# Kernel tuning notes

Hardware: AMD Instinct MI355X
Metric: run time of the kernel (lower is better)

## Reference

```python
import jax, jax.numpy as jnp
import numpy as np

HIDDEN = 4096
NH = 32          # num attention heads
NKV = 8          # num key/value heads
HD = HIDDEN // NH  # 128
THETA = 10000.0
WINDOW = 4096    # sliding window hard-coded in forward


def _rotate_half(x):
    x1, x2 = jnp.split(x, 2, axis=-1)
    return jnp.concatenate((-x2, x1), axis=-1)


def setup_inputs() -> dict:
    key = jax.random.key(0)
    ks = jax.random.split(key, 5)
    B, S = 1, 2048
    hidden_states = jax.random.normal(ks[0], (B, S, HIDDEN), jnp.float32)
    position_ids = jnp.broadcast_to(jnp.arange(S, dtype=jnp.int64), (B, S))
    s = 0.02
    q_w = jax.random.normal(ks[1], (HIDDEN, NH * HD), jnp.float32) * s
    k_w = jax.random.normal(ks[2], (HIDDEN, NKV * HD), jnp.float32) * s
    v_w = jax.random.normal(ks[3], (HIDDEN, NKV * HD), jnp.float32) * s
    o_w = jax.random.normal(ks[4], (NH * HD, HIDDEN), jnp.float32) * s
    return {"hidden_states": hidden_states, "position_ids": position_ids,
            "q_w": q_w, "k_w": k_w, "v_w": v_w, "o_w": o_w}


def reference(hidden_states, position_ids, q_w, k_w, v_w, o_w):
    B, S, _ = hidden_states.shape
    # projections (bias=False), split heads -> [B, H, S, D]
    q = (hidden_states @ q_w).reshape(B, S, NH, HD).transpose(0, 2, 1, 3)
    k = (hidden_states @ k_w).reshape(B, S, NKV, HD).transpose(0, 2, 1, 3)
    v = (hidden_states @ v_w).reshape(B, S, NKV, HD).transpose(0, 2, 1, 3)

    # rotary embedding cache (MistralRotaryEmbedding)
    inv_freq = 1.0 / (THETA ** (jnp.arange(0, HD, 2, dtype=jnp.float32) / HD))
    t = jnp.arange(S, dtype=jnp.float32)
    freqs = t[:, None] * inv_freq[None, :]           # [S, HD/2]
    emb = jnp.concatenate((freqs, freqs), axis=-1)   # [S, HD]
    cos = jnp.cos(emb)[position_ids][:, None]        # [B, 1, S, HD]
    sin = jnp.sin(emb)[position_ids][:, None]
    q = q * cos + _rotate_half(q) * sin
    k = k * cos + _rotate_half(k) * sin

    # GQA repeat_kv: [B, NKV, S, D] -> [B, NH, S, D]
    rep = NH // NKV
    k = jnp.repeat(k, rep, axis=1)
    v = jnp.repeat(v, rep, axis=1)

    # scores + sliding-window causal mask
    scale = 1.0 / np.sqrt(HD).astype(np.float32)
    w = jnp.einsum("bhqd,bhkd->bhqk", q, k) * scale  # [B, NH, S, S]
    i = jnp.arange(S)[:, None]
    j = jnp.arange(S)[None, :]
    allowed = (j <= i) & ((i - j) < WINDOW)
    neg = jnp.finfo(jnp.float32).min
    w = w + jnp.where(allowed, 0.0, neg)[None, None]

    # fp32 softmax (upcast as in HF Mistral)
    w = jax.nn.softmax(w.astype(jnp.float32), axis=-1).astype(q.dtype)

    out = jnp.einsum("bhqk,bhkd->bhqd", w, v)        # [B, NH, S, D]
    out = out.transpose(0, 2, 1, 3).reshape(B, S, NH * HD)
    return out @ o_w                                  # [B, S, HIDDEN]
```

## Files before the change

### kernel.cpp

```cpp
#include <hip/hip_runtime.h>
#include <hip/hip_bf16.h>

#define S 2048
#define HID 4096
#define NH 32
#define NKV 8
#define HD 128
#define QKVN 6144

typedef __attribute__((ext_vector_type(8))) short bf16x8;
typedef __attribute__((ext_vector_type(4))) float f32x4;
typedef __attribute__((ext_vector_type(8))) unsigned short u16x8;
typedef __attribute__((ext_vector_type(4))) unsigned short u16x4;

#define GLOAD16(src, dst)                                                        \
  __builtin_amdgcn_global_load_lds(                                              \
      (const __attribute__((address_space(1))) unsigned int*)(src),              \
      (__attribute__((address_space(3))) unsigned int*)(dst), 16, 0, 0)

__device__ __forceinline__ unsigned short f2bf(float f) {
  union { float f; unsigned u; } c; c.f = f;
  unsigned u = c.u;
  return (unsigned short)((u + 0x7FFFu + ((u >> 16) & 1u)) >> 16);
}
__device__ __forceinline__ float bf2f(unsigned short h) {
  union { unsigned u; float f; } c; c.u = ((unsigned)h) << 16;
  return c.f;
}

__global__ void convert_kernel(const float* __restrict__ in,
                               unsigned short* __restrict__ out, int n4) {
  int i = blockIdx.x * blockDim.x + threadIdx.x;
  if (i < n4) {
    float4 v = ((const float4*)in)[i];
    ushort4 o;
    o.x = f2bf(v.x); o.y = f2bf(v.y); o.z = f2bf(v.z); o.w = f2bf(v.w);
    ((ushort4*)out)[i] = o;
  }
}

__global__ void transpose_convert(const float* __restrict__ in,
                                  unsigned short* __restrict__ out, int N) {
  __shared__ float tile[32][33];
  int tx = threadIdx.x, ty = threadIdx.y;
  int n0 = blockIdx.x * 32, k0 = blockIdx.y * 32;
#pragma unroll
  for (int i = 0; i < 32; i += 8)
    tile[ty + i][tx] = in[(size_t)(k0 + ty + i) * N + n0 + tx];
  __syncthreads();
#pragma unroll
  for (int i = 0; i < 32; i += 8)
    out[(size_t)(n0 + ty + i) * HID + k0 + tx] = f2bf(tile[tx][ty + i]);
}

__device__ __forceinline__ void storeC(unsigned short* C, size_t idx, float v) { C[idx] = f2bf(v); }
__device__ __forceinline__ void storeC(float* C, size_t idx, float v) { C[idx] = v; }

template <typename OutT>
__launch_bounds__(256, 2)
__global__ void gemm_bt(const unsigned short* __restrict__ A,
                        const unsigned short* __restrict__ Bt,
                        OutT* __restrict__ C, int K, int ldc) {
  __shared__ unsigned short As[2][2][128 * 32];
  __shared__ unsigned short Bs[2][2][128 * 32];
  const int tid = threadIdx.x, lane = tid & 63, w = tid >> 6;
  const int wr = w >> 1, wc = w & 1;
  const int m0 = blockIdx.y * 128, n0 = blockIdx.x * 128;
  const int lq = lane & 15, g = lane >> 4;
  const int swz8 = (g ^ (lq & 3) ^ ((lq >> 2) & 3)) << 3;

  f32x4 acc[4][4] = {};
  const int NT = K >> 6;

  auto STAGE_PAIR = [&](int bb, int ss, int kt) {
#pragma unroll
    for (int i = 0; i < 2; ++i) {
      int ci = tid + i * 256;
      int row = ci >> 2;
      int jl = (((ci & 3) ^ (row & 3) ^ ((row >> 2) & 3))) << 3;
      GLOAD16(A + (size_t)(m0 + row) * K + kt + ss * 32 + jl, &As[bb][ss][ci * 8]);
      GLOAD16(Bt + (size_t)(n0 + row) * K + kt + ss * 32 + jl, &Bs[bb][ss][ci * 8]);
    }
  };

  STAGE_PAIR(0, 0, 0);
  STAGE_PAIR(0, 1, 0);

  for (int t = 0; t < NT; ++t) {
    const int c = t & 1;
    const bool more = (t + 1) < NT;
    const int kt1 = (t + 1) << 6;
#pragma unroll
    for (int s = 0; s < 2; ++s) {
      if (s == 0 || more) asm volatile("s_waitcnt vmcnt(4)" ::: "memory");
      else                asm volatile("s_waitcnt vmcnt(0)" ::: "memory");
      __builtin_amdgcn_s_barrier();

      bf16x8 af[4], bfr[4];
#pragma unroll
      for (int mi = 0; mi < 4; ++mi)
        af[mi] = *(const bf16x8*)&As[c][s][(wr * 64 + mi * 16 + lq) * 32 + swz8];
#pragma unroll
      for (int ni = 0; ni < 4; ++ni)
        bfr[ni] = *(const bf16x8*)&Bs[c][s][(wc * 64 + ni * 16 + lq) * 32 + swz8];

      if (more) STAGE_PAIR(c ^ 1, s, kt1);

      asm volatile("s_waitcnt lgkmcnt(0)" ::: "memory");
      __builtin_amdgcn_sched_barrier(0);
      __builtin_amdgcn_s_setprio(1);
#pragma unroll
      for (int mi = 0; mi < 4; ++mi)
#pragma unroll
        for (int ni = 0; ni < 4; ++ni)
          acc[mi][ni] = __builtin_amdgcn_mfma_f32_16x16x32_bf16(af[mi], bfr[ni], acc[mi][ni], 0, 0, 0);
      __builtin_amdgcn_s_setprio(0);
    }
  }

#pragma unroll
  for (int mi = 0; mi < 4; ++mi) {
#pragma unroll
    for (int ni = 0; ni < 4; ++ni) {
      int row = m0 + wr * 64 + mi * 16 + g * 4;
      int col = n0 + wc * 64 + ni * 16 + lq;
#pragma unroll
      for (int r = 0; r < 4; ++r)
        storeC(C, (size_t)(row + r) * ldc + col, acc[mi][ni][r]);
    }
  }
}

template <typename OutT>
__launch_bounds__(512, 1)
__global__ void gemm256_bt(const unsigned short* __restrict__ A,
                           const unsigned short* __restrict__ Bt,
                           OutT* __restrict__ C, int K, int ldc) {
  __shared__ unsigned short As[2][2][256 * 32];
  __shared__ unsigned short Bs[2][2][256 * 32];
  const int tid = threadIdx.x, lane = tid & 63, w = tid >> 6;
  const int wm = w >> 2, wn = w & 3;
  const int m0 = blockIdx.y * 256, n0 = blockIdx.x * 256;
  const int lq = lane & 15, g = lane >> 4;
  const int swz8 = (g ^ (lq & 3)) << 3;

  f32x4 acc[8][4] = {};
  const int NT = K >> 6;

  auto STAGE_PAIR = [&](int bb, int ss, int kt) {
#pragma unroll
    for (int i = 0; i < 2; ++i) {
      int ci = tid + i * 512;
      int row = ci >> 2;
      int jl = ((ci & 3) ^ (row & 3)) << 3;
      GLOAD16(A + (size_t)(m0 + row) * K + kt + ss * 32 + jl, &As[bb][ss][ci * 8]);
      GLOAD16(Bt + (size_t)(n0 + row) * K + kt + ss * 32 + jl, &Bs[bb][ss][ci * 8]);
    }
  };

  STAGE_PAIR(0, 0, 0);
  STAGE_PAIR(0, 1, 0);

  for (int t = 0; t < NT; ++t) {
    const int c = t & 1;
    const bool more = (t + 1) < NT;
    const int kt1 = (t + 1) << 6;
#pragma unroll
    for (int s = 0; s < 2; ++s) {
      if (s == 0 || more) asm volatile("s_waitcnt vmcnt(4)" ::: "memory");
      else                asm volatile("s_waitcnt vmcnt(0)" ::: "memory");
      __builtin_amdgcn_s_barrier();

      bf16x8 af[8], bf[4];
#pragma unroll
      for (int mi = 0; mi < 8; ++mi)
        af[mi] = *(const bf16x8*)&As[c][s][(wm * 128 + mi * 16 + lq) * 32 + swz8];
#pragma unroll
      for (int ni = 0; ni < 4; ++ni)
        bf[ni] = *(const bf16x8*)&Bs[c][s][(wn * 64 + ni * 16 + lq) * 32 + swz8];

      if (more) STAGE_PAIR(c ^ 1, s, kt1);

      asm volatile("s_waitcnt lgkmcnt(0)" ::: "memory");
      __builtin_amdgcn_sched_barrier(0);
      __builtin_amdgcn_s_setprio(1);
#pragma unroll
      for (int mi = 0; mi < 8; ++mi)
#pragma unroll
        for (int ni = 0; ni < 4; ++ni)
          acc[mi][ni] = __builtin_amdgcn_mfma_f32_16x16x32_bf16(af[mi], bf[ni], acc[mi][ni], 0, 0, 0);
      __builtin_amdgcn_s_setprio(0);
    }
  }

#pragma unroll
  for (int mi = 0; mi < 8; ++mi)
#pragma unroll
    for (int ni = 0; ni < 4; ++ni) {
      int row = m0 + wm * 128 + mi * 16 + g * 4;
      int col = n0 + wn * 64 + ni * 16 + lq;
#pragma unroll
      for (int r = 0; r < 4; ++r)
        storeC(C, (size_t)(row + r) * ldc + col, acc[mi][ni][r]);
    }
}

__global__ void rope_kernel(unsigned short* __restrict__ qkv) {
  int idx = blockIdx.x * blockDim.x + threadIdx.x;
  int d = idx & 63;
  int h = (idx >> 6) % (NH + NKV);
  int s = (idx >> 6) / (NH + NKV);
  size_t base = (size_t)s * QKVN + (h < NH ? h * HD : NH * HD + (h - NH) * HD);
  float invf = __expf(-(float)d * (1.0f / 64.0f) * 9.210340371976184f);
  float ang = (float)s * invf;
  float c, sn;
  __sincosf(ang, &sn, &c);
  float x1 = bf2f(qkv[base + d]);
  float x2 = bf2f(qkv[base + d + 64]);
  float o1 = x1 * c - x2 * sn;
  float o2 = x2 * c + x1 * sn;
  if (h < NH) {
    o1 *= 0.08838834764831845f;
    o2 *= 0.08838834764831845f;
  }
  qkv[base + d] = f2bf(o1);
  qkv[base + d + 64] = f2bf(o2);
}

__launch_bounds__(512, 4)
__global__ void attn_kernel(const unsigned short* __restrict__ qkv,
                            unsigned short* __restrict__ ao) {
  __shared__ unsigned short Ks[2][64 * 128];
  __shared__ unsigned short Vt[128 * 88];
  __shared__ unsigned short Ps[8][16 * 88];

  const int tid = threadIdx.x, lane = tid & 63, w = tid >> 6;
  const int b = blockIdx.x;
  const int h = blockIdx.y;
  const int qblk = (h < 16) ? (15 - b) : b;
  const int kh = h >> 2;
  const int lq = lane & 15, g = lane >> 4;
  const int qbase = qblk * 128 + w * 16;
  const size_t koff = (size_t)NH * HD + (size_t)kh * HD;
  const size_t voff = (size_t)(NH + NKV) * HD + (size_t)kh * HD;

  bf16x8 qf[4];
  {
    const unsigned short* qp = qkv + (size_t)(qbase + lq) * QKVN + (size_t)h * HD + g * 8;
#pragma unroll
    for (int ks = 0; ks < 4; ++ks) qf[ks] = *(const bf16x8*)(qp + ks * 32);
  }

  f32x4 o[8] = {};
  float m = -1e30f;
  float l = 0.f;

  auto KSTAGE = [&](int bb, int kv0) {
#pragma unroll
    for (int i = 0; i < 2; ++i) {
      int kvk = (w * 2 + i) * 4 + (lane >> 4);
      int chl = (lane & 15) ^ (kvk & 7);
      GLOAD16(qkv + (size_t)(kv0 + kvk) * QKVN + koff + chl * 8, &Ks[bb][(w * 2 + i) * 512]);
    }
  };
  const int vd0 = (tid & 31) * 4;
  const int vkv = (tid >> 5) * 4;
  u16x4 vr[4];
  auto VLOAD = [&](int kv0) {
#pragma unroll
    for (int i = 0; i < 4; ++i)
      vr[i] = *(const u16x4*)(qkv + (size_t)(kv0 + vkv + i) * QKVN + voff + vd0);
  };
  auto VWRITE = [&]() {
#pragma unroll
    for (int j = 0; j < 4; ++j) {
      const int d = vd0 + j;
      const int vswz = ((d >> 3) & 3) << 1;
      const int vcol = (((vkv >> 2) ^ vswz) << 2);
      u16x4 val = {vr[0][j], vr[1][j], vr[2][j], vr[3][j]};
      *(u16x4*)&Vt[d * 88 + vcol] = val;
    }
  };

  unsigned short* Pw = &Ps[w][0];
  const int nt = qblk * 2 + 2;

  KSTAGE(0, 0);
  VLOAD(0);
  int cur = 0;
  for (int t = 0; t < nt; ++t) {
    const int kv0 = t * 64;
    __syncthreads();
    VWRITE();
    __syncthreads();
    if (t + 1 < nt) { KSTAGE(cur ^ 1, kv0 + 64); VLOAD(kv0 + 64); }

    const int nraw = qbase + 16 - kv0;
    const int nact = nraw > 64 ? 64 : nraw;

    f32x4 sc[4];
    __builtin_amdgcn_s_setprio(1);
#pragma unroll
    for (int st = 0; st < 4; ++st) {
      if (st * 16 < nact) {
        f32x4 s = {};
#pragma unroll
        for (int ks = 0; ks < 4; ++ks) {
          const bf16x8 kf = *(const bf16x8*)
              &Ks[cur][(st * 16 + lq) * 128 + (((ks * 4 + g) ^ (lq & 7)) << 3)];
          s = __builtin_amdgcn_mfma_f32_16x16x32_bf16(kf, qf[ks], s, 0, 0, 0);
        }
        sc[st] = s;
      } else {
        sc[st] = (f32x4){-1e30f, -1e30f, -1e30f, -1e30f};
      }
    }
    __builtin_amdgcn_s_setprio(0);
    if (nraw < 79) {
      const int q = qbase + lq;
#pragma unroll
      for (int st = 0; st < 4; ++st) {
        int kv = kv0 + st * 16 + g * 4;
#pragma unroll
        for (int r = 0; r < 4; ++r)
          if (kv + r > q) sc[st][r] = -1e30f;
      }
    }

    float mn = fmaxf(fmaxf(fmaxf(sc[0][0], sc[0][1]), fmaxf(sc[0][2], sc[0][3])),
                     fmaxf(fmaxf(sc[1][0], sc[1][1]), fmaxf(sc[1][2], sc[1][3])));
    mn = fmaxf(mn, fmaxf(fmaxf(fmaxf(sc[2][0], sc[2][1]), fmaxf(sc[2][2], sc[2][3])),
                         fmaxf(fmaxf(sc[3][0], sc[3][1]), fmaxf(sc[3][2], sc[3][3]))));
    mn = fmaxf(mn, __shfl_xor(mn, 16, 64));
    mn = fmaxf(mn, __shfl_xor(mn, 32, 64));
    const bool need = __any(mn > m);
    const float m2 = fmaxf(m, mn);
    const float alpha = __expf(m - m2);
    m = m2;
    float rs = 0.f;
#pragma unroll
    for (int st = 0; st < 4; ++st)
#pragma unroll
      for (int r = 0; r < 4; ++r) {
        float p = __expf(sc[st][r] - m2);
        sc[st][r] = p;
        rs += p;
      }
    rs += __shfl_xor(rs, 16, 64);
    rs += __shfl_xor(rs, 32, 64);
    l = l * alpha + rs;

    if (need) {
      float alphaR[4];
#pragma unroll
      for (int r = 0; r < 4; ++r) alphaR[r] = __shfl(alpha, g * 4 + r, 64);
#pragma unroll
      for (int p = 0; p < 8; ++p)
#pragma unroll
        for (int r = 0; r < 4; ++r) o[p][r] *= alphaR[r];
    }

#pragma unroll
    for (int st = 0; st < 4; ++st) {
      u16x4 val = {f2bf(sc[st][0]), f2bf(sc[st][1]), f2bf(sc[st][2]), f2bf(sc[st][3])};
      *(u16x4*)&Pw[lq * 88 + st * 16 + g * 4] = val;
    }

    const int nks = nact > 0 ? (nact + 31) >> 5 : 0;
    __builtin_amdgcn_s_setprio(1);
    for (int ks = 0; ks < nks; ++ks) {
      const bf16x8 pf = *(const bf16x8*)&Pw[lq * 88 + ks * 32 + g * 8];
#pragma unroll
      for (int p = 0; p < 8; ++p) {
        const int d = p * 16 + lq;
        const int rswz = ((d >> 3) & 3) << 1;
        const int kvc = (ks * 8 + g * 2) ^ rswz;
        const bf16x8 vf = *(const bf16x8*)&Vt[d * 88 + (kvc << 2)];
        o[p] = __builtin_amdgcn_mfma_f32_16x16x32_bf16(pf, vf, o[p], 0, 0, 0);
      }
    }
    __builtin_amdgcn_s_setprio(0);

    cur ^= 1;
  }

  float invR[4];
#pragma unroll
  for (int r = 0; r < 4; ++r) invR[r] = 1.0f / __shfl(l, g * 4 + r, 64);
#pragma unroll
  for (int p = 0; p < 8; ++p)
#pragma unroll
    for (int r = 0; r < 4; ++r)
      ao[(size_t)(qbase + g * 4 + r) * (NH * HD) + (size_t)h * HD + p * 16 + lq] =
          f2bf(o[p][r] * invR[r]);
}

extern "C" void kernel_launch(void* const* d_in, const int* in_sizes, int n_in,
                              void* d_out, int out_size, void* d_ws, size_t ws_size,
                              hipStream_t stream) {
  const float* X  = (const float*)d_in[0];
  const float* qw = (const float*)d_in[2];
  const float* kw = (const float*)d_in[3];
  const float* vw = (const float*)d_in[4];
  const float* ow = (const float*)d_in[5];
  float* out = (float*)d_out;

  char* ws = (char*)d_ws;
  unsigned short* Xb  = (unsigned short*)(ws);
  unsigned short* Wt  = (unsigned short*)(ws + (size_t)(16u << 20));
  unsigned short* QKV = (unsigned short*)(ws + (size_t)(64u << 20));
  unsigned short* AO  = (unsigned short*)(ws + (size_t)(88u << 20));
  unsigned short* OWt = (unsigned short*)(ws);

  dim3 tb(32, 8);

  convert_kernel<<<(S * HID / 4 + 255) / 256, 256, 0, stream>>>(X, Xb, S * HID / 4);
  transpose_convert<<<dim3(HID / 32, HID / 32), tb, 0, stream>>>(qw, Wt, HID);
  transpose_convert<<<dim3((NKV * HD) / 32, HID / 32), tb, 0, stream>>>(kw, Wt + (size_t)(NH * HD) * HID, NKV * HD);
  transpose_convert<<<dim3((NKV * HD) / 32, HID / 32), tb, 0, stream>>>(vw, Wt + (size_t)(NH + NKV) * HD * HID, NKV * HD);
  gemm256_bt<unsigned short><<<dim3(QKVN / 256, S / 256), 512, 0, stream>>>(Xb, Wt, QKV, HID, QKVN);
  transpose_convert<<<dim3(HID / 32, HID / 32), tb, 0, stream>>>(ow, OWt, HID);
  rope_kernel<<<(S * (NH + NKV) * 64) / 256, 256, 0, stream>>>(QKV);
  attn_kernel<<<dim3(16, NH), 512, 0, stream>>>(QKV, AO);
  gemm_bt<float><<<dim3(HID / 128, S / 128), 256, 0, stream>>>(AO, OWt, out, HID, HID);
}
```

Baseline: 331.5 us.

## Restructure GEMM staging to one 64-wide K tile per buffer; use packed bf16 convert

The 256x256 GEMM now stages a whole 64-wide K tile per double buffer with an 8-way XOR swizzle. It syncs once per K tile instead of twice, which removes one barrier and one vmcnt wait per iteration. The trade-off is that the next tile's loads can only overlap with both compute halves of the current tile, and each wait is a full vmcnt(0). Separately, the attention P conversion uses the hardware v_cvt_pk_bf16_f32 instruction instead of manual rounding arithmetic.

Result: faster. 319.9 us (-3.5%).

```diff
diff --git a/kernel.cpp b/kernel.cpp
--- a/kernel.cpp
+++ b/kernel.cpp
@@ -136,61 +136,69 @@
 __global__ void gemm256_bt(const unsigned short* __restrict__ A,
                            const unsigned short* __restrict__ Bt,
                            OutT* __restrict__ C, int K, int ldc) {
-  __shared__ unsigned short As[2][2][256 * 32];
-  __shared__ unsigned short Bs[2][2][256 * 32];
+  __shared__ unsigned short As[2][256 * 64];
+  __shared__ unsigned short Bs[2][256 * 64];
   const int tid = threadIdx.x, lane = tid & 63, w = tid >> 6;
   const int wm = w >> 2, wn = w & 3;
   const int m0 = blockIdx.y * 256, n0 = blockIdx.x * 256;
   const int lq = lane & 15, g = lane >> 4;
-  const int swz8 = (g ^ (lq & 3)) << 3;
+  const int sw = lq & 7;
 
   f32x4 acc[8][4] = {};
   const int NT = K >> 6;
 
-  auto STAGE_PAIR = [&](int bb, int ss, int kt) {
-#pragma unroll
-    for (int i = 0; i < 2; ++i) {
+  auto STAGE_PAIR = [&](int bb, int kt) {
+#pragma unroll
+    for (int i = 0; i < 4; ++i) {
       int ci = tid + i * 512;
-      int row = ci >> 2;
-      int jl = ((ci & 3) ^ (row & 3)) << 3;
-      GLOAD16(A + (size_t)(m0 + row) * K + kt + ss * 32 + jl, &As[bb][ss][ci * 8]);
-      GLOAD16(Bt + (size_t)(n0 + row) * K + kt + ss * 32 + jl, &Bs[bb][ss][ci * 8]);
+      int r = ci >> 3;
+      int jl = ((ci & 7) ^ (r & 7)) << 3;
+      GLOAD16(A + (size_t)(m0 + r) * K + kt + jl, &As[bb][ci * 8]);
+      GLOAD16(Bt + (size_t)(n0 + r) * K + kt + jl, &Bs[bb][ci * 8]);
     }
   };
 
-  STAGE_PAIR(0, 0, 0);
-  STAGE_PAIR(0, 1, 0);
+  STAGE_PAIR(0, 0);
 
   for (int t = 0; t < NT; ++t) {
     const int c = t & 1;
     const bool more = (t + 1) < NT;
-    const int kt1 = (t + 1) << 6;
-#pragma unroll
-    for (int s = 0; s < 2; ++s) {
-      if (s == 0 || more) asm volatile("s_waitcnt vmcnt(4)" ::: "memory");
-      else                asm volatile("s_waitcnt vmcnt(0)" ::: "memory");
-      __builtin_amdgcn_s_barrier();
-
-      bf16x8 af[8], bf[4];
-#pragma unroll
-      for (int mi = 0; mi < 8; ++mi)
-        af[mi] = *(const bf16x8*)&As[c][s][(wm * 128 + mi * 16 + lq) * 32 + swz8];
+
+    asm volatile("s_waitcnt vmcnt(0)" ::: "memory");
+    __builtin_amdgcn_s_barrier();
+    bf16x8 af[8], bf[4];
+#pragma unroll
+    for (int mi = 0; mi < 8; ++mi)
+      af[mi] = *(const bf16x8*)&As[c][(wm * 128 + mi * 16 + lq) * 64 + ((g ^ sw) << 3)];
+#pragma unroll
+    for (int ni = 0; ni < 4; ++ni)
+      bf[ni] = *(const bf16x8*)&Bs[c][(wn * 64 + ni * 16 + lq) * 64 + ((g ^ sw) << 3)];
+    if (more) STAGE_PAIR(c ^ 1, (t + 1) << 6);
+    asm volatile("s_waitcnt lgkmcnt(0)" ::: "memory");
+    __builtin_amdgcn_sched_barrier(0);
+    __builtin_amdgcn_s_setprio(1);
+#pragma unroll
+    for (int mi = 0; mi < 8; ++mi)
 #pragma unroll
       for (int ni = 0; ni < 4; ++ni)
-        bf[ni] = *(const bf16x8*)&Bs[c][s][(wn * 64 + ni * 16 + lq) * 32 + swz8];
-
-      if (more) STAGE_PAIR(c ^ 1, s, kt1);
-
-      asm volatile("s_waitcnt lgkmcnt(0)" ::: "memory");
-      __builtin_amdgcn_sched_barrier(0);
-      __builtin_amdgcn_s_setprio(1);
-#pragma unroll
-      for (int mi = 0; mi < 8; ++mi)
-#pragma unroll
-        for (int ni = 0; ni < 4; ++ni)
-          acc[mi][ni] = __builtin_amdgcn_mfma_f32_16x16x32_bf16(af[mi], bf[ni], acc[mi][ni], 0, 0, 0);
-      __builtin_amdgcn_s_setprio(0);
-    }
+        acc[mi][ni] = __builtin_amdgcn_mfma_f32_16x16x32_bf16(af[mi], bf[ni], acc[mi][ni], 0, 0, 0);
+    __builtin_amdgcn_s_setprio(0);
+
+#pragma unroll
+    for (int mi = 0; mi < 8; ++mi)
+      af[mi] = *(const bf16x8*)&As[c][(wm * 128 + mi * 16 + lq) * 64 + (((4 + g) ^ sw) << 3)];
+#pragma unroll
+    for (int ni = 0; ni < 4; ++ni)
+      bf[ni] = *(const bf16x8*)&Bs[c][(wn * 64 + ni * 16 + lq) * 64 + (((4 + g) ^ sw) << 3)];
+    asm volatile("s_waitcnt lgkmcnt(0)" ::: "memory");
+    __builtin_amdgcn_sched_barrier(0);
+    __builtin_amdgcn_s_setprio(1);
+#pragma unroll
+    for (int mi = 0; mi < 8; ++mi)
+#pragma unroll
+      for (int ni = 0; ni < 4; ++ni)
+        acc[mi][ni] = __builtin_amdgcn_mfma_f32_16x16x32_bf16(af[mi], bf[ni], acc[mi][ni], 0, 0, 0);
+    __builtin_amdgcn_s_setprio(0);
   }
 
 #pragma unroll
@@ -362,8 +370,11 @@
 
 #pragma unroll
     for (int st = 0; st < 4; ++st) {
-      u16x4 val = {f2bf(sc[st][0]), f2bf(sc[st][1]), f2bf(sc[st][2]), f2bf(sc[st][3])};
-      *(u16x4*)&Pw[lq * 88 + st * 16 + g * 4] = val;
+      unsigned r01, r23;
+      asm("v_cvt_pk_bf16_f32 %0, %1, %2" : "=v"(r01) : "v"(sc[st][0]), "v"(sc[st][1]));
+      asm("v_cvt_pk_bf16_f32 %0, %1, %2" : "=v"(r23) : "v"(sc[st][2]), "v"(sc[st][3]));
+      unsigned* dst = (unsigned*)&Pw[lq * 88 + st * 16 + g * 4];
+      dst[0] = r01; dst[1] = r23;
     }
 
     const int nks = nact > 0 ? (nact + 31) >> 5 : 0;
```
